# Kernel tuning notes

Measured on AMD Instinct MI355X. Metric: run time of the kernel, lower is better.

The kernel has to match this reference:

```python
import jax, jax.numpy as jnp
import numpy as np

HQ, HKV, D = 16, 2, 128   # num_heads_q, num_heads_kv, head_dim
G = HQ // HKV             # q heads per kv head (repeat_interleave factor)


def setup_inputs() -> dict:
    key = jax.random.key(0)
    ks = jax.random.split(key, 6)
    B, T, C = 2, 2048, 2048
    def w(k, shape):
        return jax.random.normal(k, shape, jnp.float32) * (1.0 / np.sqrt(shape[0]).astype(np.float32))
    x = jax.random.normal(ks[0], (B, T, C), jnp.float32)
    Wq = w(ks[1], (C, HQ * D))
    Wk = w(ks[2], (C, HKV * D))
    Wv = w(ks[3], (C, HKV * D))
    Wo = w(ks[4], (HQ * D, C))
    Wg = w(ks[5], (C, HQ))
    # causal mask: True where attention is disallowed (j > i)
    mask = jnp.triu(jnp.ones((T, T), dtype=bool), k=1)[None, None]  # (1,1,T,T)
    return {"x": x, "mask": mask, "Wq": Wq, "Wk": Wk, "Wv": Wv, "Wo": Wo, "Wg": Wg}


def reference(x, mask, Wq, Wk, Wv, Wo, Wg):
    B, T, C = x.shape
    # repeat_interleave(G, dim=heads) means q head h uses kv head h // G,
    # so group q heads as (HKV, G) instead of materializing repeated K/V.
    q = (x @ Wq).reshape(B, T, HKV, G, D).transpose(0, 2, 3, 1, 4)  # (B,HKV,G,T,D)
    k = (x @ Wk).reshape(B, T, HKV, D).transpose(0, 2, 1, 3)        # (B,HKV,T,D)
    v = (x @ Wv).reshape(B, T, HKV, D).transpose(0, 2, 1, 3)        # (B,HKV,T,D)
    scale = jnp.float32(1.0 / np.sqrt(D))
    scores = jnp.einsum('bkgtd,bksd->bkgts', q, k) * scale          # (B,HKV,G,T,T)
    scores = jnp.where(mask[:, None], jnp.float32(-1e9), scores)    # causal fill
    attn = jax.nn.softmax(scores, axis=-1)
    # post-softmax sigmoid gate, one scalar per (batch, q-head, query token)
    gates = jax.nn.sigmoid(x @ Wg)                                   # (B,T,HQ)
    gates = gates.transpose(0, 2, 1).reshape(B, HKV, G, T)           # (B,HKV,G,T)
    out = jnp.einsum('bkgts,bksd->btkgd', attn * gates[..., None], v)
    out = out.reshape(B, T, HQ * D)
    return out @ Wo
```

## Files before the change

### kernel.cpp

```cpp
#include <hip/hip_runtime.h>
#include <hip/hip_bf16.h>
#include <math.h>

#define HQ 16
#define HKV 2
#define D 128
#define B_SZ 2
#define T_SZ 2048
#define C_SZ 2048
#define QKVN 2688

#define C_Q 0.12753102f
#define C_G 1.44269504f

typedef __attribute__((ext_vector_type(8))) short short8;
typedef __attribute__((ext_vector_type(4))) float floatx4;

static __device__ __forceinline__ float fexp2(float x) {
    return __builtin_amdgcn_exp2f(x);
}

static __device__ __forceinline__ unsigned short f2b(float f) {
    union { float f; unsigned u; } x; x.f = f;
    return (unsigned short)((x.u + 0x7fffu + ((x.u >> 16) & 1u)) >> 16);
}

static __device__ __forceinline__ unsigned int pk2(float a, float b) {
    float2 t; t.x = a; t.y = b;
    __hip_bfloat162 h = __float22bfloat162_rn(t);
    return *(unsigned int*)&h;
}

static __device__ __forceinline__ void load_lds16(const void* g, void* l) {
    __builtin_amdgcn_global_load_lds(
        (const __attribute__((address_space(1))) void*)g,
        (__attribute__((address_space(3))) void*)l,
        16, 0, 0);
}

static __device__ __forceinline__ void tr32(
    const float* __restrict__ in, unsigned short* __restrict__ out,
    int R, int Cc, float premul, int bx, int by, float (*t)[33])
{
    const int bc = bx * 32, br = by * 32;
    const int tid = threadIdx.x;
    const int r = tid >> 3, c4 = (tid & 7) * 4;
    float4 v = *(const float4*)(in + (size_t)(br + r) * Cc + bc + c4);
    t[r][c4 + 0] = v.x; t[r][c4 + 1] = v.y; t[r][c4 + 2] = v.z; t[r][c4 + 3] = v.w;
    __syncthreads();
    ushort4 o;
    o.x = f2b(t[c4 + 0][r] * premul); o.y = f2b(t[c4 + 1][r] * premul);
    o.z = f2b(t[c4 + 2][r] * premul); o.w = f2b(t[c4 + 3][r] * premul);
    *(ushort4*)(out + (size_t)(bc + r) * R + br + c4) = o;
}

__global__ __launch_bounds__(256) void prep_kernel(
    const float* __restrict__ x,  const float* __restrict__ Wq,
    const float* __restrict__ Wk, const float* __restrict__ Wv,
    const float* __restrict__ Wo, const float* __restrict__ Wg,
    unsigned short* __restrict__ xb, unsigned short* __restrict__ Wqkvt,
    unsigned short* __restrict__ Wot)
{
    __shared__ float t[32][33];
    const int bid = blockIdx.x;
    const int tid = threadIdx.x;
    if (bid < 4096) {
        int i = bid * 2048 + tid * 8;
        float4 a = *(const float4*)(x + i);
        float4 b = *(const float4*)(x + i + 4);
        ushort4 o0, o1;
        o0.x = f2b(a.x); o0.y = f2b(a.y); o0.z = f2b(a.z); o0.w = f2b(a.w);
        o1.x = f2b(b.x); o1.y = f2b(b.y); o1.z = f2b(b.z); o1.w = f2b(b.w);
        *(ushort4*)(xb + i) = o0;
        *(ushort4*)(xb + i + 4) = o1;
    } else if (bid < 8192) {
        int n = bid - 4096;
        tr32(Wq, Wqkvt, C_SZ, HQ * D, C_Q, n & 63, n >> 6, t);
    } else if (bid < 8704) {
        int n = bid - 8192;
        tr32(Wk, Wqkvt + (size_t)(HQ * D) * C_SZ, C_SZ, HKV * D, 1.0f, n & 7, n >> 3, t);
    } else if (bid < 9216) {
        int n = bid - 8704;
        tr32(Wv, Wqkvt + (size_t)(HQ * D + HKV * D) * C_SZ, C_SZ, HKV * D, 1.0f, n & 7, n >> 3, t);
    } else if (bid < 13312) {
        int n = bid - 9216;
        tr32(Wo, Wot, HQ * D, C_SZ, 1.0f, n & 63, n >> 6, t);
    } else {
        int k = (bid - 13312) * 256 + tid;
        const float4* wr = (const float4*)(Wg + (size_t)k * 16);
        float4 w0 = wr[0], w1 = wr[1], w2 = wr[2], w3 = wr[3];
        float w[16] = {w0.x, w0.y, w0.z, w0.w, w1.x, w1.y, w1.z, w1.w,
                       w2.x, w2.y, w2.z, w2.w, w3.x, w3.y, w3.z, w3.w};
        unsigned short* out = Wqkvt + (size_t)(HQ * D + 2 * HKV * D) * C_SZ;
        #pragma unroll
        for (int h = 0; h < 16; ++h)
            out[(size_t)h * C_SZ + k] = f2b(w[h] * C_G);
    }
}

template<int BM>
__global__ __launch_bounds__(512, 2) void gemm8p(
    const unsigned short* __restrict__ A, const unsigned short* __restrict__ Bt,
    float* __restrict__ Cf, unsigned short* __restrict__ Cb,
    unsigned short* __restrict__ Vt, int Nreal, int K, int out_bf16)
{
    constexpr int MT = BM / 32;
    constexpr int MH = MT / 2;
    constexpr int LA = BM / 128;
    constexpr int AUNIT = (BM / 2) * 64;
    constexpr int BUNIT = 8192;
    constexpr int BUF = 2 * AUNIT + 2 * BUNIT;
    constexpr int VM = LA + 4;
    __shared__ __align__(16) unsigned short SM[2][BUF];

    const int tid = threadIdx.x;
    const int lane = tid & 63, wave = tid >> 6;
    const int l15 = lane & 15, quad = lane >> 4;
    const int wm = wave >> 2, wn = wave & 3;
    const int NT = K >> 6;

    const int nwg = (int)(gridDim.x * gridDim.y);
    int flat = (int)(blockIdx.y * gridDim.x + blockIdx.x);
    const int cpx = nwg >> 3;
    flat = (flat & 7) * cpx + (flat >> 3);
    const int bm0 = (flat / (int)gridDim.x) * BM;
    const int bn0 = (flat % (int)gridDim.x) * 256;

    const int rr = tid >> 3;
    const int cb8 = ((tid & 7) ^ (rr & 7)) << 3;
    unsigned aoff[2][LA], boff[2][2];
    #pragma unroll
    for (int mh = 0; mh < 2; ++mh)
        #pragma unroll
        for (int j = 0; j < LA; ++j) {
            int row_l = j * 64 + rr;
            int grow;
            if (BM == 256) grow = bm0 + (row_l >> 6) * 128 + mh * 64 + (row_l & 63);
            else           grow = bm0 + (row_l >> 5) * 64  + mh * 32 + (row_l & 31);
            aoff[mh][j] = (unsigned)((grow * K + cb8) * 2);
        }
    #pragma unroll
    for (int nh = 0; nh < 2; ++nh)
        #pragma unroll
        for (int j = 0; j < 2; ++j) {
            int row_l = j * 64 + rr;
            int gnr = bn0 + (row_l >> 5) * 64 + nh * 32 + (row_l & 31);
            boff[nh][j] = (unsigned)((gnr * K + cb8) * 2);
        }

    floatx4 zero = {0.f, 0.f, 0.f, 0.f};
    floatx4 acc[MT][4];
    #pragma unroll
    for (int i = 0; i < MT; ++i)
        #pragma unroll
        for (int j = 0; j < 4; ++j) acc[i][j] = zero;

    auto STAGE_A = [&](int b, int mh, int t) {
        #pragma unroll
        for (int j = 0; j < LA; ++j)
            load_lds16((const char*)A + aoff[mh][j] + (size_t)t * 128,
                       &SM[b][mh * AUNIT + (j * 512 + wave * 64) * 8]);
    };
    auto STAGE_B = [&](int b, int nh, int t) {
        #pragma unroll
        for (int j = 0; j < 2; ++j)
            load_lds16((const char*)Bt + boff[nh][j] + (size_t)t * 128,
                       &SM[b][2 * AUNIT + nh * BUNIT + (j * 512 + wave * 64) * 8]);
    };

    short8 fa[MH][2], fb[4][2];
    auto RD_A = [&](int b, int mh) {
        const unsigned short* Sa = &SM[b][mh * AUNIT];
        #pragma unroll
        for (int i = 0; i < MH; ++i) {
            const int row_l = wm * (BM / 4) + i * 16 + l15;
            #pragma unroll
            for (int kk = 0; kk < 2; ++kk)
                fa[i][kk] = *(const short8*)&Sa[row_l * 64 +
                    ((((kk << 2) + quad) ^ (l15 & 7)) << 3)];
        }
    };
    auto RD_Bh = [&](int b, int nh) {
        const unsigned short* Sb = &SM[b][2 * AUNIT + nh * BUNIT];
        #pragma unroll
        for (int s = 0; s < 2; ++s) {
            const int row_l = wn * 32 + s * 16 + l15;
            #pragma unroll
            for (int kk = 0; kk < 2; ++kk)
                fb[nh * 2 + s][kk] = *(const short8*)&Sb[row_l * 64 +
                    ((((kk << 2) + quad) ^ (l15 & 7)) << 3)];
        }
    };
    auto MMQ = [&](int mh, int nh) {
        __builtin_amdgcn_s_setprio(1);
        #pragma unroll
        for (int i = 0; i < MH; ++i)
            #pragma unroll
            for (int s = 0; s < 2; ++s)
                #pragma unroll
                for (int kk = 0; kk < 2; ++kk)
                    acc[mh * MH + i][nh * 2 + s] = __builtin_amdgcn_mfma_f32_16x16x32_bf16(
                        fa[i][kk], fb[nh * 2 + s][kk], acc[mh * MH + i][nh * 2 + s], 0, 0, 0);
        __builtin_amdgcn_s_setprio(0);
    };

    STAGE_A(0, 0, 0); STAGE_B(0, 0, 0); STAGE_B(0, 1, 0); STAGE_A(0, 1, 0);
    if (NT > 1) { STAGE_A(1, 0, 1); STAGE_B(1, 0, 1); STAGE_B(1, 1, 1); }
    asm volatile("s_waitcnt vmcnt(%0)" :: "n"(VM));
    __builtin_amdgcn_s_barrier();

    #pragma unroll 2
    for (int t = 0; t < NT; ++t) {
        const int b = t & 1;
        RD_A(b, 0); RD_Bh(b, 0);
        if (t + 1 < NT) STAGE_A(b ^ 1, 1, t + 1);
        asm volatile("s_waitcnt lgkmcnt(8)");
        __builtin_amdgcn_s_barrier();
        asm volatile("s_waitcnt lgkmcnt(0)");
        MMQ(0, 0);
        __builtin_amdgcn_s_barrier();
        RD_Bh(b, 1);
        if (t + 2 < NT) STAGE_A(b, 0, t + 2);
        __builtin_amdgcn_s_barrier();
        asm volatile("s_waitcnt lgkmcnt(0)");
        MMQ(0, 1);
        __builtin_amdgcn_s_barrier();
        RD_A(b, 1);
        if (t + 2 < NT) STAGE_B(b, 0, t + 2);
        __builtin_amdgcn_s_barrier();
        asm volatile("s_waitcnt lgkmcnt(0)");
        MMQ(1, 1);
        __builtin_amdgcn_s_barrier();
        if (t + 2 < NT) {
            STAGE_B(b, 1, t + 2);
            asm volatile("s_waitcnt vmcnt(%0)" :: "n"(VM));
        } else {
            asm volatile("s_waitcnt vmcnt(0)");
        }
        __builtin_amdgcn_s_barrier();
        MMQ(1, 0);
        __builtin_amdgcn_s_barrier();
    }

    if (BM == 256 && Vt != nullptr && bn0 == 2304) {
        unsigned short (*Ct)[264] = (unsigned short(*)[264])SM;
        const int bb = bm0 >> 11;
        const int tl = bm0 & 2047;
        #pragma unroll
        for (int v = 0; v < 4; ++v) {
            __syncthreads();
            if (wn == v) {
                #pragma unroll
                for (int mt = 0; mt < MT; ++mt)
                    #pragma unroll
                    for (int nt = 0; nt < 4; ++nt)
                        #pragma unroll
                        for (int r = 0; r < 4; ++r)
                            Ct[nt * 16 + l15][wm * (BM / 2) + mt * 16 + quad * 4 + r] =
                                f2b(acc[mt][nt][r]);
            }
            __syncthreads();
            int row = tid >> 3, c0 = (tid & 7) * 32;
            unsigned short* dst = Vt + ((size_t)bb * (HKV * D) + v * 64 + row) * T_SZ
                                     + tl + c0;
            const unsigned short* src = &Ct[row][c0];
            short8 s0 = *(const short8*)(src + 0);
            short8 s1 = *(const short8*)(src + 8);
            short8 s2 = *(const short8*)(src + 16);
            short8 s3 = *(const short8*)(src + 24);
            *(short8*)(dst + 0)  = s0; *(short8*)(dst + 8)  = s1;
            *(short8*)(dst + 16) = s2; *(short8*)(dst + 24) = s3;
        }
        return;
    }

    #pragma unroll
    for (int mt = 0; mt < MT; ++mt)
        #pragma unroll
        for (int nt = 0; nt < 4; ++nt) {
            const int n = bn0 + wn * 64 + nt * 16 + l15;
            if (n < Nreal) {
                #pragma unroll
                for (int r = 0; r < 4; ++r) {
                    const int m = bm0 + wm * (BM / 2) + mt * 16 + quad * 4 + r;
                    if (out_bf16) Cb[(size_t)m * Nreal + n] = f2b(acc[mt][nt][r]);
                    else          Cf[(size_t)m * Nreal + n] = acc[mt][nt][r];
                }
            }
        }
}

__global__ __launch_bounds__(256) void attn_mfma(
    const unsigned short* __restrict__ QKV, const unsigned short* __restrict__ Vt,
    unsigned short* __restrict__ Ob)
{
    __shared__ __align__(16) unsigned short SMEM[64 * 128 + 128 * 64 + 4 * 16 * 72];
    unsigned short* Ks = SMEM;
    unsigned short* Vs = SMEM + 64 * 128;
    unsigned short* Ps = SMEM + 64 * 128 + 128 * 64;
    unsigned short* Lo = SMEM;

    const int bh = blockIdx.x;
    const int qt = (int)gridDim.y - 1 - (int)blockIdx.y;
    const int b = bh >> 4, h = bh & 15, kvh = h >> 3;
    const int tid = threadIdx.x;
    const int lane = tid & 63, w = tid >> 6;
    const int l15 = lane & 15, quad = lane >> 4;
    const int q_local = w * 16 + l15;
    const float BIAS = 32.0f;

    short8 aq[4];
    {
        const unsigned short* qp = QKV + (size_t)(b * T_SZ + qt * 64 + q_local) * QKVN
                                       + h * D + quad * 8;
        #pragma unroll
        for (int kd = 0; kd < 4; ++kd) aq[kd] = *(const short8*)(qp + kd * 32);
    }

    const unsigned short* kg[4];
    const unsigned short* vg[4];
    #pragma unroll
    for (int it = 0; it < 4; ++it) {
        int Bi = it * 256 + tid;
        int kr = Bi >> 4, kc = ((Bi & 15) ^ (kr & 15)) * 8;
        kg[it] = QKV + (size_t)(b * T_SZ + kr) * QKVN + HQ * D + kvh * D + kc;
        int vr = Bi >> 3, vc = ((Bi & 7) ^ (vr & 7)) * 8;
        vg[it] = Vt + (size_t)((b * HKV + kvh) * D + vr) * T_SZ + vc;
    }

    floatx4 zero = {0.f, 0.f, 0.f, 0.f};
    floatx4 oacc[8];
    #pragma unroll
    for (int dt = 0; dt < 8; ++dt) oacc[dt] = zero;
    float l_part = 0.f;

    for (int kt = 0; kt <= qt; ++kt) {
        __syncthreads();
        #pragma unroll
        for (int it = 0; it < 4; ++it) {
            load_lds16(kg[it] + (size_t)kt * 64 * QKVN, &Ks[(it * 256 + w * 64) * 8]);
            load_lds16(vg[it] + kt * 64,                &Vs[(it * 256 + w * 64) * 8]);
        }
        __syncthreads();

        floatx4 sacc[4];
        #pragma unroll
        for (int nt = 0; nt < 4; ++nt) sacc[nt] = zero;
        #pragma unroll
        for (int kd = 0; kd < 4; ++kd)
            #pragma unroll
            for (int nt = 0; nt < 4; ++nt) {
                short8 ak = *(const short8*)&Ks[((nt * 16 + l15) * 16 + ((kd * 4 + quad) ^ l15)) * 8];
                sacc[nt] = __builtin_amdgcn_mfma_f32_16x16x32_bf16(ak, aq[kd], sacc[nt], 0, 0, 0);
            }

        float p[4][4];
        if (kt == qt) {
            #pragma unroll
            for (int nt = 0; nt < 4; ++nt)
                #pragma unroll
                for (int r = 0; r < 4; ++r) {
                    float e = fexp2(sacc[nt][r] - BIAS);
                    p[nt][r] = (nt * 16 + quad * 4 + r > q_local) ? 0.f : e;
                }
        } else {
            #pragma unroll
            for (int nt = 0; nt < 4; ++nt)
                #pragma unroll
                for (int r = 0; r < 4; ++r)
                    p[nt][r] = fexp2(sacc[nt][r] - BIAS);
        }
        #pragma unroll
        for (int nt = 0; nt < 4; ++nt) {
            l_part += (p[nt][0] + p[nt][1]) + (p[nt][2] + p[nt][3]);
            uint2 pw;
            pw.x = pk2(p[nt][0], p[nt][1]);
            pw.y = pk2(p[nt][2], p[nt][3]);
            *(uint2*)&Ps[(w * 16 + l15) * 72 + nt * 16 + quad * 4] = pw;
        }

        #pragma unroll
        for (int kk = 0; kk < 2; ++kk) {
            short8 bp = *(const short8*)&Ps[(w * 16 + l15) * 72 + kk * 32 + quad * 8];
            #pragma unroll
            for (int dt = 0; dt < 8; ++dt) {
                short8 av = *(const short8*)&Vs[((dt * 16 + l15) * 8 + ((kk * 4 + quad) ^ (l15 & 7))) * 8];
                oacc[dt] = __builtin_amdgcn_mfma_f32_16x16x32_bf16(av, bp, oacc[dt], 0, 0, 0);
            }
        }
    }

    float l = l_part;
    l += __shfl_xor(l, 16);
    l += __shfl_xor(l, 32);

    __syncthreads();
    {
        int token = b * T_SZ + qt * 64 + q_local;
        unsigned short gl = QKV[(size_t)token * QKVN + HQ * D + HKV * D * 2 + h];
        union { unsigned u; float f; } gx; gx.u = ((unsigned)gl) << 16;
        float g = 1.0f / (1.0f + fexp2(-gx.f));
        float f = g / l;
        #pragma unroll
        for (int dt = 0; dt < 8; ++dt) {
            uint2 ov;
            ov.x = pk2(oacc[dt][0] * f, oacc[dt][1] * f);
            ov.y = pk2(oacc[dt][2] * f, oacc[dt][3] * f);
            *(uint2*)&Lo[(size_t)q_local * 136 + dt * 16 + quad * 4] = ov;
        }
    }
    __syncthreads();
    {
        int row = tid >> 2, c0 = (tid & 3) * 32;
        size_t tok = (size_t)(b * T_SZ + qt * 64 + row);
        unsigned short* op = Ob + tok * (HQ * D) + h * D + c0;
        const unsigned short* lp = &Lo[(size_t)row * 136 + c0];
        short8 v0 = *(const short8*)(lp + 0);
        short8 v1 = *(const short8*)(lp + 8);
        short8 v2 = *(const short8*)(lp + 16);
        short8 v3 = *(const short8*)(lp + 24);
        *(short8*)(op + 0)  = v0; *(short8*)(op + 8)  = v1;
        *(short8*)(op + 16) = v2; *(short8*)(op + 24) = v3;
    }
}

extern "C" void kernel_launch(void* const* d_in, const int* in_sizes, int n_in,
                              void* d_out, int out_size, void* d_ws, size_t ws_size,
                              hipStream_t stream) {
    const float* x  = (const float*)d_in[0];
    const float* Wq = (const float*)d_in[2];
    const float* Wk = (const float*)d_in[3];
    const float* Wv = (const float*)d_in[4];
    const float* Wo = (const float*)d_in[5];
    const float* Wg = (const float*)d_in[6];
    float* out = (float*)d_out;

    const size_t KB = 1ull << 10;
    char* p = (char*)d_ws;
    unsigned short* xb    = (unsigned short*)(p);
    unsigned short* Ob    = xb;
    unsigned short* Wqkvt = (unsigned short*)(p + 16384 * KB);
    unsigned short* Wot   = (unsigned short*)(p + 27136 * KB);
    unsigned short* QKV   = (unsigned short*)(p + 35328 * KB);
    unsigned short* Vt    = (unsigned short*)(p + 56832 * KB);
    const int BT = B_SZ * T_SZ;

    prep_kernel<<<dim3(13320), 256, 0, stream>>>(x, Wq, Wk, Wv, Wo, Wg, xb, Wqkvt, Wot);

    gemm8p<256><<<dim3(11, BT / 256), 512, 0, stream>>>(
        xb, Wqkvt, nullptr, QKV, Vt, QKVN, C_SZ, 1);

    attn_mfma<<<dim3(B_SZ * HQ, T_SZ / 64), 256, 0, stream>>>(QKV, Vt, Ob);

    gemm8p<128><<<dim3(8, BT / 128), 512, 0, stream>>>(
        Ob, Wot, out, nullptr, nullptr, C_SZ, HQ * D, 0);
}
```

Baseline: 280.7 us.

## Double-buffer K/V tiles and widen attention blocks to 128 queries

The attention kernel now runs 512 threads per block covering 128 query rows instead of 64, so each K/V tile loaded into LDS is shared by twice as many queries. K/V loads are double-buffered: the next tile is issued right after the barrier while the current tile is consumed, removing the second per-iteration barrier and overlapping global-to-LDS traffic with MFMA work. Waves in the lower 64-row half skip the final diagonal tile but still take part in the barriers, which leaves some imbalance. The larger LDS footprint and launch bound may lower occupancy.

```diff
diff --git a/kernel.cpp b/kernel.cpp
--- a/kernel.cpp
+++ b/kernel.cpp
@@ -290,38 +290,40 @@
         }
 }
 
-__global__ __launch_bounds__(256) void attn_mfma(
+__global__ __launch_bounds__(512) void attn_mfma(
     const unsigned short* __restrict__ QKV, const unsigned short* __restrict__ Vt,
     unsigned short* __restrict__ Ob)
 {
-    __shared__ __align__(16) unsigned short SMEM[64 * 128 + 128 * 64 + 4 * 16 * 72];
+    __shared__ __align__(16) unsigned short SMEM[2 * 8192 + 2 * 8192 + 128 * 72];
     unsigned short* Ks = SMEM;
-    unsigned short* Vs = SMEM + 64 * 128;
-    unsigned short* Ps = SMEM + 64 * 128 + 128 * 64;
+    unsigned short* Vs = SMEM + 16384;
+    unsigned short* Ps = SMEM + 32768;
     unsigned short* Lo = SMEM;
 
     const int bh = blockIdx.x;
-    const int qt = (int)gridDim.y - 1 - (int)blockIdx.y;
+    const int j = (int)gridDim.y - 1 - (int)blockIdx.y;
     const int b = bh >> 4, h = bh & 15, kvh = h >> 3;
     const int tid = threadIdx.x;
     const int lane = tid & 63, w = tid >> 6;
     const int l15 = lane & 15, quad = lane >> 4;
     const int q_local = w * 16 + l15;
+    const int qw  = j * 2 + (q_local >> 6);
+    const int qhi = j * 2 + 1;
     const float BIAS = 32.0f;
 
     short8 aq[4];
     {
-        const unsigned short* qp = QKV + (size_t)(b * T_SZ + qt * 64 + q_local) * QKVN
+        const unsigned short* qp = QKV + (size_t)(b * T_SZ + j * 128 + q_local) * QKVN
                                        + h * D + quad * 8;
         #pragma unroll
         for (int kd = 0; kd < 4; ++kd) aq[kd] = *(const short8*)(qp + kd * 32);
     }
 
-    const unsigned short* kg[4];
-    const unsigned short* vg[4];
-    #pragma unroll
-    for (int it = 0; it < 4; ++it) {
-        int Bi = it * 256 + tid;
+    const unsigned short* kg[2];
+    const unsigned short* vg[2];
+    #pragma unroll
+    for (int it = 0; it < 2; ++it) {
+        int Bi = it * 512 + tid;
         int kr = Bi >> 4, kc = ((Bi & 15) ^ (kr & 15)) * 8;
         kg[it] = QKV + (size_t)(b * T_SZ + kr) * QKVN + HQ * D + kvh * D + kc;
         int vr = Bi >> 3, vc = ((Bi & 7) ^ (vr & 7)) * 8;
@@ -334,14 +336,25 @@
     for (int dt = 0; dt < 8; ++dt) oacc[dt] = zero;
     float l_part = 0.f;
 
-    for (int kt = 0; kt <= qt; ++kt) {
+    auto STAGE = [&](int kt, int buf) {
+        #pragma unroll
+        for (int it = 0; it < 2; ++it) {
+            load_lds16(kg[it] + (size_t)kt * 64 * QKVN,
+                       &Ks[buf * 8192 + (it * 512 + w * 64) * 8]);
+            load_lds16(vg[it] + kt * 64,
+                       &Vs[buf * 8192 + (it * 512 + w * 64) * 8]);
+        }
+    };
+
+    STAGE(0, 0);
+    for (int kt = 0; kt <= qhi; ++kt) {
+        const int cur = kt & 1;
         __syncthreads();
-        #pragma unroll
-        for (int it = 0; it < 4; ++it) {
-            load_lds16(kg[it] + (size_t)kt * 64 * QKVN, &Ks[(it * 256 + w * 64) * 8]);
-            load_lds16(vg[it] + kt * 64,                &Vs[(it * 256 + w * 64) * 8]);
-        }
-        __syncthreads();
+        if (kt < qhi) STAGE(kt + 1, cur ^ 1);
+        if (kt > qw) continue;
+
+        const unsigned short* Kc = Ks + cur * 8192;
+        const unsigned short* Vc = Vs + cur * 8192;
 
         floatx4 sacc[4];
         #pragma unroll
@@ -350,18 +363,19 @@
         for (int kd = 0; kd < 4; ++kd)
             #pragma unroll
             for (int nt = 0; nt < 4; ++nt) {
-                short8 ak = *(const short8*)&Ks[((nt * 16 + l15) * 16 + ((kd * 4 + quad) ^ l15)) * 8];
+                short8 ak = *(const short8*)&Kc[((nt * 16 + l15) * 16 + ((kd * 4 + quad) ^ l15)) * 8];
                 sacc[nt] = __builtin_amdgcn_mfma_f32_16x16x32_bf16(ak, aq[kd], sacc[nt], 0, 0, 0);
             }
 
         float p[4][4];
-        if (kt == qt) {
+        if (kt == qw) {
+            const int qm = q_local & 63;
             #pragma unroll
             for (int nt = 0; nt < 4; ++nt)
                 #pragma unroll
                 for (int r = 0; r < 4; ++r) {
                     float e = fexp2(sacc[nt][r] - BIAS);
-                    p[nt][r] = (nt * 16 + quad * 4 + r > q_local) ? 0.f : e;
+                    p[nt][r] = (nt * 16 + quad * 4 + r > qm) ? 0.f : e;
                 }
         } else {
             #pragma unroll
@@ -384,7 +398,7 @@
             short8 bp = *(const short8*)&Ps[(w * 16 + l15) * 72 + kk * 32 + quad * 8];
             #pragma unroll
             for (int dt = 0; dt < 8; ++dt) {
-                short8 av = *(const short8*)&Vs[((dt * 16 + l15) * 8 + ((kk * 4 + quad) ^ (l15 & 7))) * 8];
+                short8 av = *(const short8*)&Vc[((dt * 16 + l15) * 8 + ((kk * 4 + quad) ^ (l15 & 7))) * 8];
                 oacc[dt] = __builtin_amdgcn_mfma_f32_16x16x32_bf16(av, bp, oacc[dt], 0, 0, 0);
             }
         }
@@ -396,7 +410,7 @@
 
     __syncthreads();
     {
-        int token = b * T_SZ + qt * 64 + q_local;
+        int token = b * T_SZ + j * 128 + q_local;
         unsigned short gl = QKV[(size_t)token * QKVN + HQ * D + HKV * D * 2 + h];
         union { unsigned u; float f; } gx; gx.u = ((unsigned)gl) << 16;
         float g = 1.0f / (1.0f + fexp2(-gx.f));
@@ -412,7 +426,7 @@
     __syncthreads();
     {
         int row = tid >> 2, c0 = (tid & 3) * 32;
-        size_t tok = (size_t)(b * T_SZ + qt * 64 + row);
+        size_t tok = (size_t)(b * T_SZ + j * 128 + row);
         unsigned short* op = Ob + tok * (HQ * D) + h * D + c0;
         const unsigned short* lp = &Lo[(size_t)row * 136 + c0];
         short8 v0 = *(const short8*)(lp + 0);
@@ -450,7 +464,7 @@
     gemm8p<256><<<dim3(11, BT / 256), 512, 0, stream>>>(
         xb, Wqkvt, nullptr, QKV, Vt, QKVN, C_SZ, 1);
 
-    attn_mfma<<<dim3(B_SZ * HQ, T_SZ / 64), 256, 0, stream>>>(QKV, Vt, Ob);
+    attn_mfma<<<dim3(B_SZ * HQ, T_SZ / 128), 512, 0, stream>>>(QKV, Vt, Ob);
 
     gemm8p<128><<<dim3(8, BT / 128), 512, 0, stream>>>(
         Ob, Wot, out, nullptr, nullptr, C_SZ, HQ * D, 0);
```

Result: no change. 278.7 us (-0.7%).
